# Kernel optimization log

Hardware: AMD Instinct MI355X
Metric: run time of the kernel (lower is better)

## Reference

```python
import jax, jax.numpy as jnp
import numpy as np

B, C_IN, T = 32, 64, 512
N_FILT, K, GN_G = 256, 9, 8
H = 512
N_CLS = 50
EPS = 1e-5


def _group_norm(x, gamma, beta, groups, eps=EPS):
    # x: (B, C, T)
    b, c, t = x.shape
    xg = x.reshape(b, groups, c // groups, t)
    mu = xg.mean(axis=(2, 3), keepdims=True)
    var = xg.var(axis=(2, 3), keepdims=True)
    xn = ((xg - mu) * jax.lax.rsqrt(var + eps)).reshape(b, c, t)
    return xn * gamma[None, :, None] + beta[None, :, None]


def _lstm_layer(x, w_ih, w_hh, b):
    # x: (B, T, Din); w_ih: (4H, Din); w_hh: (4H, H); b: (4H,) (b_ih+b_hh fused)
    # Precompute input projections for all timesteps (one big GEMM).
    xg = jnp.einsum('btd,gd->btg', x, w_ih) + b  # (B, T, 4H)
    h_dim = w_hh.shape[1]
    bsz = x.shape[0]

    def step(carry, xt):
        h, c = carry
        gates = xt + h @ w_hh.T  # (B, 4H)
        i, f, g, o = jnp.split(gates, 4, axis=-1)  # PyTorch gate order i,f,g,o
        i = jax.nn.sigmoid(i)
        f = jax.nn.sigmoid(f)
        g = jnp.tanh(g)
        o = jax.nn.sigmoid(o)
        c = f * c + i * g
        h = o * jnp.tanh(c)
        return (h, c), h

    h0 = jnp.zeros((bsz, h_dim), x.dtype)
    _, hs = jax.lax.scan(step, (h0, h0), jnp.swapaxes(xg, 0, 1))  # (T, B, H)
    return jnp.swapaxes(hs, 0, 1)  # (B, T, H)


def setup_inputs() -> dict:
    key = jax.random.key(0)
    ks = jax.random.split(key, 16)
    sc = lambda fan: 1.0 / np.sqrt(fan)
    inp = {
        'x_emg': jax.random.normal(ks[0], (B, C_IN, T), jnp.float32),
        'conv_w': jax.random.normal(ks[1], (N_FILT, C_IN, K), jnp.float32) * sc(C_IN * K),
        'gn_gamma': jnp.ones((N_FILT,), jnp.float32),
        'gn_beta': jnp.zeros((N_FILT,), jnp.float32),
        'head_w': jax.random.normal(ks[2], (N_CLS, H), jnp.float32) * sc(H),
        'head_b': jnp.zeros((N_CLS,), jnp.float32),
    }
    dins = [N_FILT, H, H]
    for l in range(3):
        inp[f'w_ih{l+1}'] = jax.random.normal(ks[3 + 3 * l], (4 * H, dins[l]), jnp.float32) * sc(dins[l])
        inp[f'w_hh{l+1}'] = jax.random.normal(ks[4 + 3 * l], (4 * H, H), jnp.float32) * sc(H)
        # forget-gate bias init to 1 (b_ih+b_hh fused -> 2.0 in slot [H:2H])
        b = jnp.zeros((4 * H,), jnp.float32).at[H:2 * H].set(2.0)
        inp[f'b{l+1}'] = b
    return inp


def reference(x_emg, conv_w, gn_gamma, gn_beta, w_ih1, w_hh1, b1,
              w_ih2, w_hh2, b2, w_ih3, w_hh3, b3, head_w, head_b):
    # Conv1d (no bias), padding=k//2 -> same length
    h = jax.lax.conv_general_dilated(
        x_emg, conv_w, window_strides=(1,), padding=[(K // 2, K // 2)],
        dimension_numbers=('NCH', 'OIH', 'NCH'))  # (B, F, T)
    h = jax.nn.relu(_group_norm(h, gn_gamma, gn_beta, GN_G))
    h = jnp.transpose(h, (0, 2, 1))  # (B, T, F)
    h1 = _lstm_layer(h, w_ih1, w_hh1, b1)
    h2 = _lstm_layer(h1, w_ih2, w_hh2, b2)
    h3 = _lstm_layer(h2, w_ih3, w_hh3, b3)
    feat = h3.mean(axis=1)  # (B, H) mean-pool over time
    return feat @ head_w.T + head_b  # (B, n_classes)
```

## Files before the change

kernel.cpp:

```cpp
#include <hip/hip_runtime.h>
#include <stdint.h>
#include <math.h>

#define B_SZ 32
#define C_IN 64
#define T_SZ 512
#define NFILT 256
#define KW 9
#define H_SZ 512
#define N_CLS 50

typedef __bf16 bf16x8 __attribute__((ext_vector_type(8)));
typedef float f32x16 __attribute__((ext_vector_type(16)));

#define MFMA32(a, b, c) __builtin_amdgcn_mfma_f32_32x32x16_bf16((a), (b), (c), 0, 0, 0)

__device__ __forceinline__ bf16x8 ld_frag_sys(const __bf16* p) {
  union { unsigned long long u[2]; bf16x8 v; } r;
  r.u[0] = __hip_atomic_load((const unsigned long long*)p, __ATOMIC_RELAXED,
                             __HIP_MEMORY_SCOPE_SYSTEM);
  r.u[1] = __hip_atomic_load((const unsigned long long*)(p + 4), __ATOMIC_RELAXED,
                             __HIP_MEMORY_SCOPE_SYSTEM);
  return r.v;
}
__device__ __forceinline__ void st_u32_sys(unsigned* p, unsigned v) {
  __hip_atomic_store(p, v, __ATOMIC_RELAXED, __HIP_MEMORY_SCOPE_SYSTEM);
}
__device__ __forceinline__ unsigned* flagp(unsigned* flags, int layer, int t) {
  return flags + (((size_t)layer * T_SZ + t) << 4);
}
__device__ __forceinline__ void wait_flag(const unsigned* f) {
  while (__hip_atomic_load(f, __ATOMIC_RELAXED, __HIP_MEMORY_SCOPE_SYSTEM) < 32u)
    __builtin_amdgcn_s_sleep(1);
}

__global__ __launch_bounds__(256, 1) void conv_gn_kernel(
    const float* __restrict__ x, const float* __restrict__ w,
    const float* __restrict__ gamma, const float* __restrict__ beta,
    __bf16* __restrict__ x1h, __bf16* __restrict__ x1l) {
  extern __shared__ float xs[];
  const int b = blockIdx.x >> 3;
  const int g = blockIdx.x & 7;
  const int tid = threadIdx.x;
  const float* xb = x + (size_t)b * (C_IN * T_SZ);
  for (int i = tid; i < C_IN * T_SZ / 4; i += 256) {
    int c = i >> 7;
    int t4 = (i & 127) << 2;
    float4 v = *(const float4*)(xb + c * T_SZ + t4);
    *(float4*)(&xs[c * 520 + 4 + t4]) = v;
  }
  for (int i = tid; i < C_IN * 8; i += 256) {
    int c = i >> 3, j = i & 7;
    xs[c * 520 + (j < 4 ? j : 512 + j)] = 0.f;
  }
  __syncthreads();
  const int fl = tid & 31;
  const int f = g * 32 + fl;
  const int t0 = (tid >> 5) << 6;
  float acc[64];
#pragma unroll
  for (int t = 0; t < 64; ++t) acc[t] = 0.f;
  const float* wf = w + (size_t)f * (C_IN * KW);
  for (int c = 0; c < C_IN; ++c) {
    float wr[9];
#pragma unroll
    for (int k = 0; k < 9; ++k) wr[k] = wf[c * 9 + k];
    float xr[72];
    const float* xrow = &xs[c * 520 + t0];
#pragma unroll
    for (int j = 0; j < 72; ++j) xr[j] = xrow[j];
#pragma unroll
    for (int t = 0; t < 64; ++t) {
      float s = acc[t];
#pragma unroll
      for (int k = 0; k < 9; ++k) s = fmaf(xr[t + k], wr[k], s);
      acc[t] = s;
    }
  }
  float s1 = 0.f, s2 = 0.f;
#pragma unroll
  for (int t = 0; t < 64; ++t) { s1 += acc[t]; s2 = fmaf(acc[t], acc[t], s2); }
#pragma unroll
  for (int off = 32; off > 0; off >>= 1) {
    s1 += __shfl_down(s1, off);
    s2 += __shfl_down(s2, off);
  }
  float* red = xs + 64 * 520;
  if ((tid & 63) == 0) { red[tid >> 6] = s1; red[4 + (tid >> 6)] = s2; }
  __syncthreads();
  if (tid == 0) {
    float a = red[0] + red[1] + red[2] + red[3];
    float q = red[4] + red[5] + red[6] + red[7];
    float mu = a * (1.f / 16384.f);
    float var = q * (1.f / 16384.f) - mu * mu;
    red[8] = mu;
    red[9] = 1.f / sqrtf(var + 1e-5f);
  }
  __syncthreads();
  const float mu = red[8], inv = red[9];
  const float ga = gamma[f], be = beta[f];
#pragma unroll
  for (int t = 0; t < 64; ++t) {
    float v = (acc[t] - mu) * inv * ga + be;
    v = fmaxf(v, 0.f);
    __bf16 hh = (__bf16)v;
    __bf16 hl = (__bf16)(v - (float)hh);
    size_t idx = ((size_t)b * T_SZ + (t0 + t)) * NFILT + f;
    x1h[idx] = hh;
    x1l[idx] = hl;
  }
}

__global__ __launch_bounds__(256, 1) void lstm_scan_kernel(
    const float* __restrict__ wih1, const float* __restrict__ whh1, const float* __restrict__ bb1,
    const float* __restrict__ wih2, const float* __restrict__ whh2, const float* __restrict__ bb2,
    const float* __restrict__ wih3, const float* __restrict__ whh3, const float* __restrict__ bb3,
    const __bf16* __restrict__ x1h, const __bf16* __restrict__ x1l,
    __bf16* __restrict__ xAh, __bf16* __restrict__ xAl,
    __bf16* __restrict__ xBh, __bf16* __restrict__ xBl,
    __bf16* __restrict__ hbase,
    float* __restrict__ feat, unsigned* __restrict__ flags) {
  __shared__ float gl[4][32][72];

  const int wg = blockIdx.x;
  const int layer = wg >> 5;
  const int wgl = wg & 31;
  const int tid = threadIdx.x;
  const int lane = tid & 63;
  const int wave = tid >> 6;

  const float* wih = layer == 0 ? wih1 : (layer == 1 ? wih2 : wih3);
  const float* whh = layer == 0 ? whh1 : (layer == 1 ? whh2 : whh3);
  const float* bias = layer == 0 ? bb1 : (layer == 1 ? bb2 : bb3);
  const int Din = layer == 0 ? NFILT : H_SZ;
  const __bf16* xinh = layer == 0 ? x1h : (layer == 1 ? xAh : xBh);
  const __bf16* xinl = layer == 0 ? x1l : (layer == 1 ? xAl : xBl);
  __bf16* xoh = layer == 0 ? xAh : xBh;
  __bf16* xol = layer == 0 ? xAl : xBl;

  const bool is_x = (wave >= 2);
  const int kbase = (wave & 1) << 8;
  const bool dead = (layer == 0) && (wave == 3);

  bf16x8 wfh[2][16], wfl[2][16];
  {
    const float* wsrc = is_x ? wih : whh;
    const int wk = is_x ? Din : H_SZ;
#pragma unroll
    for (int nt = 0; nt < 2; ++nt) {
      const int nloc = nt * 32 + (lane & 31);
      const int orow = (nloc >> 4) * 512 + wgl * 16 + (nloc & 15);
      const float* wrow = wsrc + (size_t)orow * wk;
#pragma unroll
      for (int kt = 0; kt < 16; ++kt) {
        const int k0 = kbase + kt * 16 + ((lane >> 5) << 3);
        bf16x8 hi, lo;
#pragma unroll
        for (int e = 0; e < 8; ++e) {
          float v = 0.f;
          if (!is_x || (k0 + e) < Din) v = wrow[k0 + e];
          __bf16 h = (__bf16)v;
          hi[e] = h;
          lo[e] = (__bf16)(v - (float)h);
        }
        wfh[nt][kt] = hi;
        wfl[nt][kt] = lo;
      }
    }
  }

  const int cm = tid >> 3;
  const int cq = tid & 7;
  const int ul0 = cq * 2;
  const int unit0 = wgl * 16 + ul0;
  float cb[4][2];
#pragma unroll
  for (int gg = 0; gg < 4; ++gg) {
    cb[gg][0] = bias[gg * 512 + unit0];
    cb[gg][1] = bias[gg * 512 + unit0 + 1];
  }
  float cst[2] = {0.f, 0.f};
  float hsum[2] = {0.f, 0.f};

  const int arow = lane & 31;
  const int agrp = (lane >> 5) << 3;

  for (int t = 0; t < T_SZ; ++t) {
    f32x16 acc[2][2] = {};
    if (!is_x) {
      if (t > 0) {
        wait_flag(flagp(flags, layer, t - 1));
        const int rp = (t - 1) & 1;
        const __bf16* hb = hbase + ((size_t)(rp * 3 + layer) * 2) * 16384;
        const __bf16* ahb = hb + (size_t)arow * 512;
        const __bf16* alb = hb + 16384 + (size_t)arow * 512;
#pragma unroll
        for (int kt = 0; kt < 16; ++kt) {
          const int k0 = kbase + kt * 16 + agrp;
          const bf16x8 ah = ld_frag_sys(ahb + k0);
          const bf16x8 al = ld_frag_sys(alb + k0);
          const int p = kt & 1;
#pragma unroll
          for (int nt = 0; nt < 2; ++nt) {
            f32x16 a = acc[nt][p];
            a = MFMA32(ah, wfh[nt][kt], a);
            a = MFMA32(al, wfh[nt][kt], a);
            a = MFMA32(ah, wfl[nt][kt], a);
            acc[nt][p] = a;
          }
        }
      }
    } else if (!dead) {
      if (layer > 0) wait_flag(flagp(flags, layer - 1, t));
      const __bf16* ahb = xinh + ((size_t)arow * T_SZ + t) * Din;
      const __bf16* alb = xinl + ((size_t)arow * T_SZ + t) * Din;
#pragma unroll
      for (int kt = 0; kt < 16; ++kt) {
        const int k0 = kbase + kt * 16 + agrp;
        const bf16x8 ah = *(const bf16x8*)(ahb + k0);
        const bf16x8 al = *(const bf16x8*)(alb + k0);
        const int p = kt & 1;
#pragma unroll
        for (int nt = 0; nt < 2; ++nt) {
          f32x16 a = acc[nt][p];
          a = MFMA32(ah, wfh[nt][kt], a);
          a = MFMA32(al, wfh[nt][kt], a);
          a = MFMA32(ah, wfl[nt][kt], a);
          acc[nt][p] = a;
        }
      }
    }
#pragma unroll
    for (int nt = 0; nt < 2; ++nt) {
      const f32x16 v = acc[nt][0] + acc[nt][1];
      const int n = nt * 32 + (lane & 31);
#pragma unroll
      for (int r = 0; r < 16; ++r) {
        const int m = (r & 3) + ((r >> 2) << 3) + ((lane >> 5) << 2);
        gl[wave][m][n] = v[r];
      }
    }
    __syncthreads();
    {
      __bf16* hw = hbase + ((size_t)((t & 1) * 3 + layer) * 2) * 16384;
      float hv[2];
#pragma unroll
      for (int j = 0; j < 2; ++j) {
        float gv[4];
#pragma unroll
        for (int gg = 0; gg < 4; ++gg) {
          gv[gg] = gl[0][cm][gg * 16 + ul0 + j] + gl[1][cm][gg * 16 + ul0 + j] +
                   gl[2][cm][gg * 16 + ul0 + j] + gl[3][cm][gg * 16 + ul0 + j] + cb[gg][j];
        }
        const float ig = 1.f / (1.f + expf(-gv[0]));
        const float fg = 1.f / (1.f + expf(-gv[1]));
        const float gc = tanhf(gv[2]);
        const float og = 1.f / (1.f + expf(-gv[3]));
        const float c_ = fg * cst[j] + ig * gc;
        cst[j] = c_;
        hv[j] = og * tanhf(c_);
      }
      union { __bf16 b[2]; unsigned u; } ph, pl;
      ph.b[0] = (__bf16)hv[0];
      ph.b[1] = (__bf16)hv[1];
      pl.b[0] = (__bf16)(hv[0] - (float)ph.b[0]);
      pl.b[1] = (__bf16)(hv[1] - (float)ph.b[1]);
      st_u32_sys((unsigned*)(hw + (size_t)cm * 512 + unit0), ph.u);
      st_u32_sys((unsigned*)(hw + 16384 + (size_t)cm * 512 + unit0), pl.u);
      if (layer < 2) {
        const size_t xo = ((size_t)cm * T_SZ + t) * 512 + unit0;
        st_u32_sys((unsigned*)(xoh + xo), ph.u);
        st_u32_sys((unsigned*)(xol + xo), pl.u);
      } else {
        hsum[0] += hv[0];
        hsum[1] += hv[1];
      }
    }
    __syncthreads();
    if (tid == 0)
      __hip_atomic_fetch_add(flagp(flags, layer, t), 1u, __ATOMIC_RELAXED,
                             __HIP_MEMORY_SCOPE_SYSTEM);
  }
  if (layer == 2) {
    feat[(size_t)cm * 512 + unit0] = hsum[0] * (1.f / 512.f);
    feat[(size_t)cm * 512 + unit0 + 1] = hsum[1] * (1.f / 512.f);
  }
}

__global__ void head_kernel(const float* __restrict__ feat, const float* __restrict__ hw,
                            const float* __restrict__ hb, float* __restrict__ out) {
  const int bi = blockIdx.x;
  const int b = bi / N_CLS;
  const int n = bi % N_CLS;
  const int lane = threadIdx.x;
  float s = 0.f;
  for (int j = lane; j < H_SZ; j += 64) s = fmaf(feat[b * H_SZ + j], hw[n * H_SZ + j], s);
#pragma unroll
  for (int off = 32; off > 0; off >>= 1) s += __shfl_down(s, off);
  if (lane == 0) out[b * N_CLS + n] = s + hb[n];
}

extern "C" void kernel_launch(void* const* d_in, const int* in_sizes, int n_in,
                              void* d_out, int out_size, void* d_ws, size_t ws_size,
                              hipStream_t stream) {
  const float* x_emg = (const float*)d_in[0];
  const float* conv_w = (const float*)d_in[1];
  const float* gn_g = (const float*)d_in[2];
  const float* gn_b = (const float*)d_in[3];
  const float* head_w = (const float*)d_in[4];
  const float* head_b = (const float*)d_in[5];
  const float* wih1 = (const float*)d_in[6];
  const float* whh1 = (const float*)d_in[7];
  const float* b1 = (const float*)d_in[8];
  const float* wih2 = (const float*)d_in[9];
  const float* whh2 = (const float*)d_in[10];
  const float* b2 = (const float*)d_in[11];
  const float* wih3 = (const float*)d_in[12];
  const float* whh3 = (const float*)d_in[13];
  const float* b3 = (const float*)d_in[14];
  float* out = (float*)d_out;

  char* p = (char*)d_ws;
  auto alloc = [&](size_t sz) {
    char* r = p;
    p += (sz + 255) & ~(size_t)255;
    return r;
  };
  unsigned* flags = (unsigned*)alloc((size_t)3 * T_SZ * 64);
  __bf16* x1h = (__bf16*)alloc((size_t)B_SZ * T_SZ * NFILT * 2);
  __bf16* x1l = (__bf16*)alloc((size_t)B_SZ * T_SZ * NFILT * 2);
  __bf16* xAh = (__bf16*)alloc((size_t)B_SZ * T_SZ * H_SZ * 2);
  __bf16* xAl = (__bf16*)alloc((size_t)B_SZ * T_SZ * H_SZ * 2);
  __bf16* xBh = (__bf16*)alloc((size_t)B_SZ * T_SZ * H_SZ * 2);
  __bf16* xBl = (__bf16*)alloc((size_t)B_SZ * T_SZ * H_SZ * 2);
  __bf16* hbase = (__bf16*)alloc((size_t)2 * 3 * 2 * 16384 * 2);
  float* feat = (float*)alloc((size_t)B_SZ * H_SZ * 4);

  hipMemsetAsync(flags, 0, (size_t)3 * T_SZ * 64, stream);
  conv_gn_kernel<<<dim3(256), dim3(256), (64 * 520 + 16) * 4, stream>>>(
      x_emg, conv_w, gn_g, gn_b, x1h, x1l);
  lstm_scan_kernel<<<dim3(96), dim3(256), 0, stream>>>(
      wih1, whh1, b1, wih2, whh2, b2, wih3, whh3, b3,
      x1h, x1l, xAh, xAl, xBh, xBl, hbase, feat, flags);
  head_kernel<<<dim3(B_SZ * N_CLS), dim3(64), 0, stream>>>(feat, head_w, head_b, out);
}
```

Before: 4.888 ms.

## Replace per-step atomic counters with per-block progress words and use fast gate math

Drops the per-timestep atomic fetch-add flag counters. Each workgroup now stores its own progress counter, and waiters poll all 32 counters of a layer in parallel across lanes with a wave vote and no sleep. This is meant to cut the latency of the inter-block barrier in the serial LSTM recurrence. It also swaps expf/tanhf for sigmoid and tanh built from hardware exp2 and reciprocal, which shortens the per-step gate math at some accuracy cost and with saturation edge cases in tanh. Busy polling without sleep raises memory traffic while blocks wait.

```diff
diff --git a/kernel.cpp b/kernel.cpp
--- a/kernel.cpp
+++ b/kernel.cpp
@@ -15,6 +15,13 @@
 
 #define MFMA32(a, b, c) __builtin_amdgcn_mfma_f32_32x32x16_bf16((a), (b), (c), 0, 0, 0)
 
+__device__ __forceinline__ float fast_sigmoid(float x) {
+  return __builtin_amdgcn_rcpf(1.f + __builtin_amdgcn_exp2f(-1.442695040889f * x));
+}
+__device__ __forceinline__ float fast_tanh(float x) {
+  return 1.f - 2.f * __builtin_amdgcn_rcpf(1.f + __builtin_amdgcn_exp2f(2.885390081778f * x));
+}
+
 __device__ __forceinline__ bf16x8 ld_frag_sys(const __bf16* p) {
   union { unsigned long long u[2]; bf16x8 v; } r;
   r.u[0] = __hip_atomic_load((const unsigned long long*)p, __ATOMIC_RELAXED,
@@ -26,12 +33,12 @@
 __device__ __forceinline__ void st_u32_sys(unsigned* p, unsigned v) {
   __hip_atomic_store(p, v, __ATOMIC_RELAXED, __HIP_MEMORY_SCOPE_SYSTEM);
 }
-__device__ __forceinline__ unsigned* flagp(unsigned* flags, int layer, int t) {
-  return flags + (((size_t)layer * T_SZ + t) << 4);
-}
-__device__ __forceinline__ void wait_flag(const unsigned* f) {
-  while (__hip_atomic_load(f, __ATOMIC_RELAXED, __HIP_MEMORY_SCOPE_SYSTEM) < 32u)
-    __builtin_amdgcn_s_sleep(1);
+__device__ __forceinline__ void wait_prog(const unsigned* prog, unsigned target) {
+  const unsigned* p = prog + (threadIdx.x & 31);
+  while (true) {
+    unsigned v = __hip_atomic_load(p, __ATOMIC_RELAXED, __HIP_MEMORY_SCOPE_SYSTEM);
+    if (__all((int)(v >= target))) break;
+  }
 }
 
 __global__ __launch_bounds__(256, 1) void conv_gn_kernel(
@@ -119,7 +126,7 @@
     __bf16* __restrict__ xAh, __bf16* __restrict__ xAl,
     __bf16* __restrict__ xBh, __bf16* __restrict__ xBl,
     __bf16* __restrict__ hbase,
-    float* __restrict__ feat, unsigned* __restrict__ flags) {
+    float* __restrict__ feat, unsigned* __restrict__ prog) {
   __shared__ float gl[4][32][72];
 
   const int wg = blockIdx.x;
@@ -137,6 +144,8 @@
   const __bf16* xinl = layer == 0 ? x1l : (layer == 1 ? xAl : xBl);
   __bf16* xoh = layer == 0 ? xAh : xBh;
   __bf16* xol = layer == 0 ? xAl : xBl;
+  unsigned* prog_self = prog + layer * 32;
+  const unsigned* prog_up = prog + (layer - 1) * 32;
 
   const bool is_x = (wave >= 2);
   const int kbase = (wave & 1) << 8;
@@ -189,7 +198,7 @@
     f32x16 acc[2][2] = {};
     if (!is_x) {
       if (t > 0) {
-        wait_flag(flagp(flags, layer, t - 1));
+        wait_prog(prog_self, (unsigned)t);
         const int rp = (t - 1) & 1;
         const __bf16* hb = hbase + ((size_t)(rp * 3 + layer) * 2) * 16384;
         const __bf16* ahb = hb + (size_t)arow * 512;
@@ -211,7 +220,7 @@
         }
       }
     } else if (!dead) {
-      if (layer > 0) wait_flag(flagp(flags, layer - 1, t));
+      if (layer > 0) wait_prog(prog_up, (unsigned)(t + 1));
       const __bf16* ahb = xinh + ((size_t)arow * T_SZ + t) * Din;
       const __bf16* alb = xinl + ((size_t)arow * T_SZ + t) * Din;
 #pragma unroll
@@ -252,13 +261,13 @@
           gv[gg] = gl[0][cm][gg * 16 + ul0 + j] + gl[1][cm][gg * 16 + ul0 + j] +
                    gl[2][cm][gg * 16 + ul0 + j] + gl[3][cm][gg * 16 + ul0 + j] + cb[gg][j];
         }
-        const float ig = 1.f / (1.f + expf(-gv[0]));
-        const float fg = 1.f / (1.f + expf(-gv[1]));
-        const float gc = tanhf(gv[2]);
-        const float og = 1.f / (1.f + expf(-gv[3]));
+        const float ig = fast_sigmoid(gv[0]);
+        const float fg = fast_sigmoid(gv[1]);
+        const float gc = fast_tanh(gv[2]);
+        const float og = fast_sigmoid(gv[3]);
         const float c_ = fg * cst[j] + ig * gc;
         cst[j] = c_;
-        hv[j] = og * tanhf(c_);
+        hv[j] = og * fast_tanh(c_);
       }
       union { __bf16 b[2]; unsigned u; } ph, pl;
       ph.b[0] = (__bf16)hv[0];
@@ -277,9 +286,7 @@
       }
     }
     __syncthreads();
-    if (tid == 0)
-      __hip_atomic_fetch_add(flagp(flags, layer, t), 1u, __ATOMIC_RELAXED,
-                             __HIP_MEMORY_SCOPE_SYSTEM);
+    if (tid == 0) st_u32_sys(prog_self + wgl, (unsigned)(t + 1));
   }
   if (layer == 2) {
     feat[(size_t)cm * 512 + unit0] = hsum[0] * (1.f / 512.f);
@@ -326,7 +333,7 @@
     p += (sz + 255) & ~(size_t)255;
     return r;
   };
-  unsigned* flags = (unsigned*)alloc((size_t)3 * T_SZ * 64);
+  unsigned* prog = (unsigned*)alloc(512);
   __bf16* x1h = (__bf16*)alloc((size_t)B_SZ * T_SZ * NFILT * 2);
   __bf16* x1l = (__bf16*)alloc((size_t)B_SZ * T_SZ * NFILT * 2);
   __bf16* xAh = (__bf16*)alloc((size_t)B_SZ * T_SZ * H_SZ * 2);
@@ -336,11 +343,11 @@
   __bf16* hbase = (__bf16*)alloc((size_t)2 * 3 * 2 * 16384 * 2);
   float* feat = (float*)alloc((size_t)B_SZ * H_SZ * 4);
 
-  hipMemsetAsync(flags, 0, (size_t)3 * T_SZ * 64, stream);
+  hipMemsetAsync(prog, 0, 512, stream);
   conv_gn_kernel<<<dim3(256), dim3(256), (64 * 520 + 16) * 4, stream>>>(
       x_emg, conv_w, gn_g, gn_b, x1h, x1l);
   lstm_scan_kernel<<<dim3(96), dim3(256), 0, stream>>>(
       wih1, whh1, b1, wih2, whh2, b2, wih3, whh3, b3,
-      x1h, x1l, xAh, xAl, xBh, xBl, hbase, feat, flags);
+      x1h, x1l, xAh, xAl, xBh, xBl, hbase, feat, prog);
   head_kernel<<<dim3(B_SZ * N_CLS), dim3(64), 0, stream>>>(feat, head_w, head_b, out);
 }
```

After: 4.500 ms. -8.0%, faster.
